# Optimization experiments

Measured on AMD Instinct MI355X. Metric: run time of the kernel, lower is better.

The kernel has to match this reference:

```python
import jax, jax.numpy as jnp
import numpy as np

N = 32768      # tokens
E = 2048       # embedding_dim
V = 256        # vq_dim
K = 256        # codebook size (levels=[256] -> single level, log2 K = 8)
HID = 1024     # condition MLP hidden dim
LOG2K = 8      # log2_num_embeddings
N_MID = 4      # condition_layer - 2 middle blocks
BN_EPS = 1e-5


def _normalize(x):
    return x / (jnp.linalg.norm(x, axis=-1, keepdims=True) + 1e-6)


def _bn(x, g, b):
    # BatchNorm1d, training-mode batch statistics over the codebook rows
    m = x.mean(0)
    v = x.var(0)
    return g * (x - m) * jax.lax.rsqrt(v + BN_EPS) + b


def _codebook(w0, b0, g0, be0, wm, bm, gm, bem, wL, bL):
    # get_bvectors(8, 256): binary expansion of 0..255, width 8 (no pad needed)
    ints = jnp.arange(K)
    bits = ((ints[:, None] >> jnp.arange(LOG2K - 1, -1, -1)[None, :]) & 1).astype(jnp.float32)
    x = jax.nn.relu(_bn(bits @ w0 + b0, g0, be0))
    for i in range(N_MID):
        x = jax.nn.relu(_bn(x @ wm[i] + bm[i], gm[i], bem[i]))
    return x @ wL + bL  # [K, V]


def setup_inputs() -> dict:
    key = jax.random.key(0)
    ks = jax.random.split(key, 8)
    def lin(k, fan_in, shape):
        return (jax.random.normal(k, shape, jnp.float32) / np.sqrt(fan_in)).astype(jnp.float32)
    return {
        "h_in": jax.random.normal(ks[0], (N, E), jnp.float32),
        "temp": jnp.array([0.3], jnp.float32),
        "proj_w": lin(ks[1], E, (E, V)), "proj_b": jnp.zeros((V,), jnp.float32),
        "pinv_w": lin(ks[2], V, (V, E)), "pinv_b": jnp.zeros((E,), jnp.float32),
        "w0": lin(ks[3], LOG2K, (LOG2K, HID)), "b0": jnp.zeros((HID,), jnp.float32),
        "g0": jnp.ones((HID,), jnp.float32), "be0": jnp.zeros((HID,), jnp.float32),
        "wm": lin(ks[4], HID, (N_MID, HID, HID)), "bm": jnp.zeros((N_MID, HID), jnp.float32),
        "gm": jnp.ones((N_MID, HID), jnp.float32), "bem": jnp.zeros((N_MID, HID), jnp.float32),
        "wL": lin(ks[5], HID, (HID, V)), "bL": jnp.zeros((V,), jnp.float32),
    }


def reference(h_in, temp, proj_w, proj_b, pinv_w, pinv_b,
              w0, b0, g0, be0, wm, bm, gm, bem, wL, bL):
    # forward(h_in, mode='eval', temperature=1, level=256); levels=[256] -> idx_all=1
    h = _normalize(h_in @ proj_w + proj_b)                          # proj + sphere normalize, [N, V]
    embed = _normalize(_codebook(w0, b0, g0, be0, wm, bm, gm, bem, wL, bL))  # [K, V]

    # attention(): distance logits with temperature-scaled detached term
    sim = h @ embed.T                                               # [N, K]
    alpha = 1.0 / temp ** 2
    distances = -2.0 * (alpha - 1.0) * jax.lax.stop_gradient(sim) - 2.0 * sim
    A = jax.nn.softmax(-distances, axis=1)                          # [N, K]

    k_code, k_p = jax.random.split(jax.random.key(42))
    code = jax.random.categorical(k_code, -distances, axis=-1)      # multinomial(A, 1), [N]
    onehot = jax.nn.one_hot(code, K, dtype=A.dtype)
    c = onehot * (1.0 - A) + (1.0 - onehot) * (-A)
    A2 = A + jax.lax.stop_gradient(c)                               # fwd value == onehot
    h_vq = h + A2 @ embed - jax.lax.stop_gradient(h)                # straight-through quantize
    vq_loss = jnp.linalg.norm(h_vq - h, axis=-1).mean()             # idx_all == 1

    # select = (0 < p) & (p < 1) since idx=0, idx_all=1
    p = jax.random.uniform(k_p, (h.shape[0],))
    select = (0.0 < p) & (p < 1.0)
    quantized = h_vq * select[:, None].astype(h_vq.dtype)
    probs = A * select[:, None].astype(A.dtype)
    vq_code = code * select.astype(code.dtype)

    quantized_inv = quantized @ pinv_w + pinv_b                     # [N, E]
    return quantized_inv, vq_code, quantized, probs, vq_loss
```

## Files before the change

### kernel.cpp

```cpp
#include <hip/hip_runtime.h>
#include <hip/hip_bf16.h>
#include <stdint.h>
#include <stddef.h>

#ifndef PARTITIONABLE
#define PARTITIONABLE 1
#endif

typedef __attribute__((ext_vector_type(8))) short short8;
typedef __attribute__((ext_vector_type(4))) short short4v;
typedef __attribute__((ext_vector_type(4))) float f32x4;

__host__ __device__ __forceinline__ uint32_t rotl32(uint32_t x, int d){ return (x<<d)|(x>>(32-d)); }

__host__ __device__ __forceinline__ void tf4(uint32_t&x0, uint32_t&x1, int r0,int r1,int r2,int r3){
  x0+=x1; x1=rotl32(x1,r0); x1^=x0;
  x0+=x1; x1=rotl32(x1,r1); x1^=x0;
  x0+=x1; x1=rotl32(x1,r2); x1^=x0;
  x0+=x1; x1=rotl32(x1,r3); x1^=x0;
}
__host__ __device__ __forceinline__ void threefry2x32(uint32_t k0,uint32_t k1,uint32_t x0,uint32_t x1,
                                                      uint32_t&y0,uint32_t&y1){
  uint32_t ks2 = k0^k1^0x1BD11BDAu;
  x0+=k0; x1+=k1;
  tf4(x0,x1,13,15,26,6);  x0+=k1;  x1+=ks2+1u;
  tf4(x0,x1,17,29,16,24); x0+=ks2; x1+=k0+2u;
  tf4(x0,x1,13,15,26,6);  x0+=k0;  x1+=k1+3u;
  tf4(x0,x1,17,29,16,24); x0+=k1;  x1+=ks2+4u;
  tf4(x0,x1,13,15,26,6);  x0+=ks2; x1+=k0+5u;
  y0=x0; y1=x1;
}

__device__ __forceinline__ uint32_t random_bits32(uint32_t k0,uint32_t k1,uint32_t idx, uint32_t half){
#if PARTITIONABLE
  uint32_t y0,y1; threefry2x32(k0,k1, 0u, idx, y0,y1);
  (void)half;
  return y0 ^ y1;
#else
  uint32_t y0,y1;
  if (idx < half) { threefry2x32(k0,k1, idx, idx+half, y0,y1); return y0; }
  else            { threefry2x32(k0,k1, idx-half, idx, y0,y1); return y1; }
#endif
}

__device__ __forceinline__ unsigned short bf16_rne(float x){
  unsigned u = __float_as_uint(x);
  unsigned r = (u + 0x7FFFu + ((u>>16)&1u)) >> 16;
  return (unsigned short)r;
}
__device__ __forceinline__ float bf16_tof(unsigned short h){
  return __uint_as_float(((unsigned)h)<<16);
}
__device__ __forceinline__ void split8(const float* src, short8& hi, short8& lo){
  #pragma unroll
  for (int e=0;e<8;e++){
    unsigned short h = bf16_rne(src[e]);
    hi[e] = (short)h;
    lo[e] = (short)bf16_rne(src[e] - bf16_tof(h));
  }
}
__device__ __forceinline__ void split4(const float* src, short4v& hi, short4v& lo){
  #pragma unroll
  for (int e=0;e<4;e++){
    unsigned short h = bf16_rne(src[e]);
    hi[e] = (short)h;
    lo[e] = (short)bf16_rne(src[e] - bf16_tof(h));
  }
}

__device__ __forceinline__ void gll16(const void* g, void* l){
  __builtin_amdgcn_global_load_lds(
      (const __attribute__((address_space(1))) unsigned int*)g,
      (__attribute__((address_space(3))) unsigned int*)l, 16, 0, 0);
}

__device__ __forceinline__ void mk1_gemm(const float* __restrict__ A, int lda,
                                         const unsigned short* __restrict__ packB,
                                         int K, char* smem, f32x4 (&acc)[2][4]){
  const int tid=threadIdx.x, lane=tid&63, wv=tid>>6;
  const int wr=wv>>2, wc=wv&3;
  const int arow=tid>>3, aseg=tid&7, swA=(arow>>1)&3;
  unsigned short* Ahi=(unsigned short*)smem;
  unsigned short* Alo=(unsigned short*)(smem+4096);
  unsigned short* Bhi=(unsigned short*)(smem+8192);
  unsigned short* Blo=(unsigned short*)(smem+24576);
  const int NT=K/32;
  const int sA = arow*32 + ((aseg>>1)^swA)*8 + (aseg&1)*4;
  const int seg = wv*2;

  float4 av = *(const float4*)(A + (size_t)arow*lda + aseg*4);
  for(int t=0;t<NT;t++){
    __syncthreads();
    {
      float af[4]={av.x,av.y,av.z,av.w}; short4v vh,vl; split4(af,vh,vl);
      *(short4v*)&Ahi[sA]=vh; *(short4v*)&Alo[sA]=vl;
      const unsigned short* src = packB + (size_t)t*16384;
      #pragma unroll
      for(int q=0;q<2;q++){
        gll16(src + (seg+q)*512 + lane*8,        (char*)Bhi + (seg+q)*1024);
        gll16(src + 8192 + (seg+q)*512 + lane*8, (char*)Blo + (seg+q)*1024);
      }
      if (t+1<NT) av = *(const float4*)(A + (size_t)arow*lda + (t+1)*32 + aseg*4);
    }
    __syncthreads();
    short8 ah[2],al[2],bh[4],bl[4];
    const int kg=lane>>4;
    #pragma unroll
    for(int i=0;i<2;i++){
      const int r = wr*32 + i*16 + (lane&15);
      const int offA = r*32 + ((kg ^ ((r>>1)&3))*8);
      ah[i]=*(const short8*)&Ahi[offA]; al[i]=*(const short8*)&Alo[offA];
    }
    #pragma unroll
    for(int j=0;j<4;j++){
      const int c = wc*64 + j*16 + (lane&15);
      const int offB = c*32 + ((kg ^ ((c>>1)&3))*8);
      bh[j]=*(const short8*)&Bhi[offB]; bl[j]=*(const short8*)&Blo[offB];
    }
    #pragma unroll
    for(int i=0;i<2;i++)
      #pragma unroll
      for(int j=0;j<4;j++){
        acc[i][j]=__builtin_amdgcn_mfma_f32_16x16x32_bf16(ah[i],bh[j],acc[i][j],0,0,0);
        acc[i][j]=__builtin_amdgcn_mfma_f32_16x16x32_bf16(ah[i],bl[j],acc[i][j],0,0,0);
        acc[i][j]=__builtin_amdgcn_mfma_f32_16x16x32_bf16(al[i],bh[j],acc[i][j],0,0,0);
      }
  }
}

__global__ __launch_bounds__(256) void pack_w_kernel(const float* __restrict__ W,
                                                     unsigned short* __restrict__ pack){
  const int t = blockIdx.x>>2, s = blockIdx.x&3, c = threadIdx.x;
  const int g = s ^ ((c>>1)&3);
  const float* p = W + (size_t)(t*32 + g*8)*256 + c;
  float bf[8];
  #pragma unroll
  for(int e=0;e<8;e++) bf[e]=p[(size_t)e*256];
  short8 h,l; split8(bf,h,l);
  unsigned short* dst = pack + (size_t)t*16384 + c*32 + s*8;
  *(short8*)dst = h;
  *(short8*)(dst+8192) = l;
}

__device__ __forceinline__ void bn_block_t(float (&acc)[4], int col0,
                                           const float* __restrict__ gma,
                                           const float* __restrict__ bta,
                                           float* __restrict__ Yt,
                                           float* Zs, float* red, float* mcol, float* vcol){
  const int r = threadIdx.x;
  #pragma unroll
  for (int j=0;j<4;j++) Zs[r*5+j] = acc[j];
  __syncthreads();
  if (r < 16){
    const int rl = r & 3, j = r >> 2;
    float s = 0.f;
    for (int rr=rl; rr<256; rr+=4) s += Zs[rr*5+j];
    red[rl*4+j] = s;
  }
  __syncthreads();
  if (r < 4)
    mcol[r] = (red[0*4+r]+red[1*4+r]+red[2*4+r]+red[3*4+r]) * (1.0f/256.0f);
  __syncthreads();
  if (r < 16){
    const int rl = r & 3, j = r >> 2;
    const float m = mcol[j];
    float s2 = 0.f;
    for (int rr=rl; rr<256; rr+=4){ float d = Zs[rr*5+j]-m; s2 += d*d; }
    red[rl*4+j] = s2;
  }
  __syncthreads();
  if (r < 4)
    vcol[r] = (red[0*4+r]+red[1*4+r]+red[2*4+r]+red[3*4+r]) * (1.0f/256.0f);
  __syncthreads();
  #pragma unroll
  for (int j=0;j<4;j++){
    const int c = col0 + j;
    const float scale = gma[c] * rsqrtf(vcol[j] + 1e-5f);
    const float sh = bta[c];
    const float v = (acc[j]-mcol[j])*scale + sh;
    Yt[(size_t)c*256 + r] = v > 0.f ? v : 0.f;
  }
}

__global__ __launch_bounds__(256) void mlp_layer_kernel(
    const float* __restrict__ Xt, const float* __restrict__ W,
    const float* __restrict__ bias,
    const float* __restrict__ gma, const float* __restrict__ bta,
    float* __restrict__ Yt){
  __shared__ float Ws[1024*4];
  __shared__ float Zs[256*5];
  __shared__ float red[16], mcol[4], vcol[4];
  const int r = threadIdx.x;
  const int col0 = blockIdx.x*4;
  #pragma unroll
  for (int q=0;q<4;q++){
    const int k = q*256 + r;
    const float4 wv = *(const float4*)&W[(size_t)k*1024 + col0];
    *(float4*)&Ws[k*4] = wv;
  }
  __syncthreads();
  float acc[4] = {0.f,0.f,0.f,0.f};
  #pragma unroll 8
  for (int k=0;k<1024;k++){
    const float a = Xt[(size_t)k*256 + r];
    const float4 wv = *(const float4*)&Ws[k*4];
    acc[0] += a*wv.x; acc[1] += a*wv.y; acc[2] += a*wv.z; acc[3] += a*wv.w;
  }
  #pragma unroll
  for (int j=0;j<4;j++) acc[j] += bias[col0+j];
  bn_block_t(acc, col0, gma, bta, Yt, Zs, red, mcol, vcol);
}

__global__ __launch_bounds__(256) void mlp_l0t_kernel(
    const float* __restrict__ w0, const float* __restrict__ b0,
    const float* __restrict__ g0, const float* __restrict__ be0,
    float* __restrict__ Yt){
  __shared__ float Zs[256*5];
  __shared__ float red[16], mcol[4], vcol[4];
  const int i = threadIdx.x;
  const int col0 = blockIdx.x*4;
  float acc[4];
  #pragma unroll
  for (int j=0;j<4;j++) acc[j] = b0[col0+j];
  #pragma unroll
  for (int jj=0;jj<8;jj++){
    if ((i >> (7-jj)) & 1){
      #pragma unroll
      for (int j=0;j<4;j++) acc[j] += w0[jj*1024 + col0 + j];
    }
  }
  bn_block_t(acc, col0, g0, be0, Yt, Zs, red, mcol, vcol);
}

__global__ __launch_bounds__(256) void mlp_tail_kernel(
    const float* __restrict__ Xt,
    const float* __restrict__ wL, const float* __restrict__ bL,
    const float* __restrict__ pinv_w, const float* __restrict__ pinv_b,
    float* __restrict__ embed, unsigned short* __restrict__ packE,
    float* __restrict__ Epp){
  __shared__ float xrow[1024];
  __shared__ float erow[256];
  __shared__ float wsum[4];
  const int n = blockIdx.x, t = threadIdx.x;
  #pragma unroll
  for (int q=0;q<4;q++) xrow[q*256+t] = Xt[(size_t)(q*256+t)*256 + n];
  __syncthreads();
  float acc = 0.f;
  #pragma unroll 8
  for (int k=0;k<1024;k++) acc += xrow[k] * wL[(size_t)k*256 + t];
  acc += bL[t];
  const int lane = t & 63, wv = t >> 6;
  float v = acc*acc;
  #pragma unroll
  for (int o=32;o;o>>=1) v += __shfl_xor(v,o);
  if (lane==0) wsum[wv]=v;
  __syncthreads();
  const float total = wsum[0]+wsum[1]+wsum[2]+wsum[3];
  const float inv = 1.0f/(sqrtf(total)+1e-6f);
  const float y = acc*inv;
  embed[(size_t)n*256+t] = y;
  erow[t] = y;
  {
    unsigned short h = bf16_rne(y);
    unsigned short l = bf16_rne(y - bf16_tof(h));
    const int tt=t>>5, kk=t&31, g=kk>>3, e=kk&7, s=g^((n>>1)&3);
    unsigned short* d = packE + (size_t)tt*16384 + n*32 + s*8 + e;
    d[0] = h; d[8192] = l;
  }
  __syncthreads();
  float a8[8] = {0.f,0.f,0.f,0.f,0.f,0.f,0.f,0.f};
  #pragma unroll 4
  for (int k=0;k<256;k++){
    const float ev = erow[k];
    const float4 w0v = *(const float4*)&pinv_w[(size_t)k*2048 + t*8];
    const float4 w1v = *(const float4*)&pinv_w[(size_t)k*2048 + t*8 + 4];
    a8[0] += ev*w0v.x; a8[1] += ev*w0v.y; a8[2] += ev*w0v.z; a8[3] += ev*w0v.w;
    a8[4] += ev*w1v.x; a8[5] += ev*w1v.y; a8[6] += ev*w1v.z; a8[7] += ev*w1v.w;
  }
  #pragma unroll
  for (int j=0;j<8;j++) a8[j] += pinv_b[t*8+j];
  float4* dst = (float4*)(Epp + (size_t)n*2048 + t*8);
  dst[0] = (float4){a8[0],a8[1],a8[2],a8[3]};
  dst[1] = (float4){a8[4],a8[5],a8[6],a8[7]};
}

__global__ __launch_bounds__(512) void proj_norm_kernel(
    const float* __restrict__ A, const unsigned short* __restrict__ packW,
    const float* __restrict__ bias, float* __restrict__ Hn, int K){
  __shared__ char smem[40960];
  f32x4 acc[2][4];
  #pragma unroll
  for (int i=0;i<2;i++)
    #pragma unroll
    for (int j=0;j<4;j++) acc[i][j] = (f32x4){0.f,0.f,0.f,0.f};
  const int bm = blockIdx.x * 64;
  mk1_gemm(A + (size_t)bm*K, K, packW, K, smem, acc);
  __syncthreads();

  const int tid = threadIdx.x, lane = tid&63, wv = tid>>6;
  const int wr = wv>>2, wc = wv&3;
  float* ns = (float*)smem;
  #pragma unroll
  for (int j=0;j<4;j++){
    const int c = wc*64 + j*16 + (lane&15);
    const float bb = bias[c];
    #pragma unroll
    for (int i=0;i<2;i++)
      #pragma unroll
      for (int reg=0;reg<4;reg++) acc[i][j][reg] += bb;
  }
  #pragma unroll
  for (int i=0;i<2;i++)
    #pragma unroll
    for (int reg=0;reg<4;reg++){
      float p = acc[i][0][reg]*acc[i][0][reg] + acc[i][1][reg]*acc[i][1][reg]
              + acc[i][2][reg]*acc[i][2][reg] + acc[i][3][reg]*acc[i][3][reg];
      #pragma unroll
      for (int o=1;o<16;o<<=1) p += __shfl_xor(p, o);
      if ((lane&15)==0) ns[wc*64 + wr*32 + i*16 + (lane>>4)*4 + reg] = p;
    }
  __syncthreads();
  #pragma unroll
  for (int i=0;i<2;i++){
    const int rl = wr*32 + i*16 + (lane>>4)*4;
    #pragma unroll
    for (int reg=0;reg<4;reg++){
      const int r = rl + reg;
      const float tot = ns[0*64+r]+ns[1*64+r]+ns[2*64+r]+ns[3*64+r];
      const float inv = 1.0f/(sqrtf(tot)+1e-6f);
      const size_t grow = (size_t)(bm + r);
      #pragma unroll
      for (int j=0;j<4;j++){
        const int c = wc*64 + j*16 + (lane&15);
        Hn[grow*256 + c] = acc[i][j][reg]*inv;
      }
    }
  }
}

__global__ __launch_bounds__(512) void sim_sample_kernel(
    const float* __restrict__ Hn, const unsigned short* __restrict__ packE,
    const float* __restrict__ embed, const float* __restrict__ temp,
    float* __restrict__ probs, float* __restrict__ codef,
    float* __restrict__ quant, float* __restrict__ norms,
    const float* __restrict__ Epp, const float* __restrict__ pinv_b,
    float* __restrict__ q_inv,
    uint32_t kc0, uint32_t kc1, uint32_t kp0, uint32_t kp1){
  __shared__ char smem[40960];
  f32x4 acc[2][4];
  #pragma unroll
  for (int i=0;i<2;i++)
    #pragma unroll
    for (int j=0;j<4;j++) acc[i][j] = (f32x4){0.f,0.f,0.f,0.f};
  const int bm = blockIdx.x * 64;
  mk1_gemm(Hn + (size_t)bm*256, 256, packE, 256, smem, acc);
  __syncthreads();

  float* redf = (float*)smem;
  int*   redi = (int*)(smem+1024);
  float* smax = (float*)(smem+2048);
  float* ssum = (float*)(smem+2304);
  float* ssel = (float*)(smem+2560);
  int*  scode = (int*)(smem+2816);

  const int tid = threadIdx.x, lane = tid&63, wv = tid>>6;
  const int wr = wv>>2, wc = wv&3;
  const float tv = temp[0];
  const float alpha = 1.0f/(tv*tv);
  #pragma unroll
  for (int i=0;i<2;i++)
    #pragma unroll
    for (int j=0;j<4;j++)
      #pragma unroll
      for (int reg=0;reg<4;reg++){
        const float s = acc[i][j][reg];
        const float dist = -2.0f*(alpha-1.0f)*s - 2.0f*s;
        acc[i][j][reg] = -dist;
      }
  #pragma unroll
  for (int i=0;i<2;i++)
    #pragma unroll
    for (int reg=0;reg<4;reg++){
      float m = fmaxf(fmaxf(acc[i][0][reg], acc[i][1][reg]),
                      fmaxf(acc[i][2][reg], acc[i][3][reg]));
      #pragma unroll
      for (int o=1;o<16;o<<=1) m = fmaxf(m, __shfl_xor(m, o));
      if ((lane&15)==0) redf[wc*64 + wr*32 + i*16 + (lane>>4)*4 + reg] = m;
    }
  __syncthreads();
  if (tid < 64)
    smax[tid] = fmaxf(fmaxf(redf[0*64+tid], redf[1*64+tid]), fmaxf(redf[2*64+tid], redf[3*64+tid]));
  __syncthreads();
  #pragma unroll
  for (int i=0;i<2;i++)
    #pragma unroll
    for (int reg=0;reg<4;reg++){
      const int r = wr*32 + i*16 + (lane>>4)*4 + reg;
      const float m = smax[r];
      float p = expf(acc[i][0][reg]-m) + expf(acc[i][1][reg]-m)
              + expf(acc[i][2][reg]-m) + expf(acc[i][3][reg]-m);
      #pragma unroll
      for (int o=1;o<16;o<<=1) p += __shfl_xor(p, o);
      if ((lane&15)==0) redf[wc*64 + r] = p;
    }
  __syncthreads();
  if (tid < 64){
    ssum[tid] = redf[0*64+tid]+redf[1*64+tid]+redf[2*64+tid]+redf[3*64+tid];
    const uint32_t pb = random_bits32(kp0,kp1,(uint32_t)(bm+tid), 16384u);
    const float pf = __uint_as_float((pb>>9) | 0x3f800000u) - 1.0f;
    ssel[tid] = (pf > 0.0f) ? 1.0f : 0.0f;
  }
  __syncthreads();
  #pragma unroll
  for (int i=0;i<2;i++)
    #pragma unroll
    for (int reg=0;reg<4;reg++){
      const int r = wr*32 + i*16 + (lane>>4)*4 + reg;
      const uint32_t grow = (uint32_t)(bm + r);
      float zb = -1e38f; int ib = 0x7fffffff;
      #pragma unroll
      for (int j=0;j<4;j++){
        const int c = wc*64 + j*16 + (lane&15);
        const uint32_t bits = random_bits32(kc0,kc1, grow*256u + (uint32_t)c, 4194304u);
        const float f = __uint_as_float((bits>>9) | 0x3f800000u) - 1.0f;
        const float TINY = 1.17549435082228751e-38f;
        const float u = fmaxf(TINY, f + TINY);
        const float g = -logf(-logf(u));
        const float z = acc[i][j][reg] + g;
        if (z > zb || (z == zb && c < ib)){ zb = z; ib = c; }
      }
      #pragma unroll
      for (int o=1;o<16;o<<=1){
        const float zo = __shfl_xor(zb, o); const int io = __shfl_xor(ib, o);
        if (zo > zb || (zo == zb && io < ib)){ zb = zo; ib = io; }
      }
      if ((lane&15)==0){ redf[wc*64 + r] = zb; redi[wc*64 + r] = ib; }
    }
  __syncthreads();
  if (tid < 64){
    float zb = redf[0*64+tid]; int ib = redi[0*64+tid];
    #pragma unroll
    for (int w=1; w<4; w++)
      if (redf[w*64+tid] > zb || (redf[w*64+tid] == zb && redi[w*64+tid] < ib)){
        zb = redf[w*64+tid]; ib = redi[w*64+tid];
      }
    scode[tid] = ib;
  }
  __syncthreads();
  #pragma unroll
  for (int i=0;i<2;i++)
    #pragma unroll
    for (int reg=0;reg<4;reg++){
      const int r = wr*32 + i*16 + (lane>>4)*4 + reg;
      const size_t grow = (size_t)(bm + r);
      const float m = smax[r], sum = ssum[r], sel = ssel[r];
      const int code = scode[r];
      float p2 = 0.f;
      #pragma unroll
      for (int j=0;j<4;j++){
        const int c = wc*64 + j*16 + (lane&15);
        const float e = expf(acc[i][j][reg] - m);
        probs[grow*256 + c] = (e/sum) * sel;
        const float ev = embed[(size_t)code*256 + c];
        quant[grow*256 + c] = ev * sel;
        const float d = ev - Hn[grow*256 + c];
        p2 += d*d;
      }
      #pragma unroll
      for (int o=1;o<16;o<<=1) p2 += __shfl_xor(p2, o);
      if ((lane&15)==0) redf[wc*64 + r] = p2;
    }
  __syncthreads();
  if (tid < 64){
    norms[bm+tid] = sqrtf(redf[0*64+tid]+redf[1*64+tid]+redf[2*64+tid]+redf[3*64+tid]);
    codef[bm+tid] = (float)scode[tid] * ssel[tid];
  }
  #pragma unroll
  for (int rr=0; rr<8; rr++){
    const int r = wv*8 + rr;
    const int code = scode[r];
    const float sel = ssel[r];
    const float4* s4 = (const float4*)((sel != 0.0f) ? (Epp + (size_t)code*2048) : pinv_b);
    float4* dst = (float4*)(q_inv + (size_t)(bm + r)*2048);
    #pragma unroll
    for (int q=0;q<8;q++) dst[q*64 + lane] = s4[q*64 + lane];
  }
}

__global__ __launch_bounds__(256) void loss_kernel(const float* __restrict__ norms,
                                                   float* __restrict__ outp){
  const int t = threadIdx.x;
  float s = 0.f;
  for (int i=t;i<32768;i+=256) s += norms[i];
  #pragma unroll
  for (int o=32;o;o>>=1) s += __shfl_xor(s,o);
  __shared__ float wred[4];
  if ((t&63)==0) wred[t>>6]=s;
  __syncthreads();
  if (t==0) outp[0] = (wred[0]+wred[1]+wred[2]+wred[3]) * (1.0f/32768.0f);
}

extern "C" void kernel_launch(void* const* d_in, const int* in_sizes, int n_in,
                              void* d_out, int out_size, void* d_ws, size_t ws_size,
                              hipStream_t stream){
  const float* h_in  = (const float*)d_in[0];
  const float* temp  = (const float*)d_in[1];
  const float* proj_w= (const float*)d_in[2];
  const float* proj_b= (const float*)d_in[3];
  const float* pinv_w= (const float*)d_in[4];
  const float* pinv_b= (const float*)d_in[5];
  const float* w0 = (const float*)d_in[6];
  const float* b0 = (const float*)d_in[7];
  const float* g0 = (const float*)d_in[8];
  const float* be0= (const float*)d_in[9];
  const float* wm = (const float*)d_in[10];
  const float* bm = (const float*)d_in[11];
  const float* gm = (const float*)d_in[12];
  const float* bem= (const float*)d_in[13];
  const float* wL = (const float*)d_in[14];
  const float* bL = (const float*)d_in[15];

  float* out = (float*)d_out;
  float* q_inv  = out;
  float* o_code = out + 67108864;
  float* o_quant= out + 67141632;
  float* o_probs= out + 75530240;
  float* o_loss = out + 83918848;

  float* ws = (float*)d_ws;
  float* Hn     = ws + 0;
  float* XtA    = ws + 8388608;
  float* XtB    = ws + 8650752;
  float* embed  = ws + 8912896;
  float* norms  = ws + 8978432;
  float* Epp    = ws + 9076736;
  unsigned short* packW = (unsigned short*)(ws + 9601024);
  unsigned short* packE = (unsigned short*)(ws + 10125312);

  uint32_t kc0,kc1,kp0,kp1;
#if PARTITIONABLE
  threefry2x32(0u,42u, 0u,0u, kc0,kc1);
  threefry2x32(0u,42u, 0u,1u, kp0,kp1);
#else
  { uint32_t a0,b0w,a1,b1w;
    threefry2x32(0u,42u, 0u,2u, a0,b0w);
    threefry2x32(0u,42u, 1u,3u, a1,b1w);
    kc0=a0; kc1=a1; kp0=b0w; kp1=b1w; }
#endif

  pack_w_kernel<<<256,256,0,stream>>>(proj_w, packW);

  proj_norm_kernel<<<512,512,0,stream>>>(h_in, packW, proj_b, Hn, 2048);

  mlp_l0t_kernel<<<256,256,0,stream>>>(w0, b0, g0, be0, XtA);
  mlp_layer_kernel<<<256,256,0,stream>>>(XtA, wm + 0*1048576, bm + 0*1024, gm + 0*1024, bem + 0*1024, XtB);
  mlp_layer_kernel<<<256,256,0,stream>>>(XtB, wm + 1*1048576, bm + 1*1024, gm + 1*1024, bem + 1*1024, XtA);
  mlp_layer_kernel<<<256,256,0,stream>>>(XtA, wm + 2*1048576, bm + 2*1024, gm + 2*1024, bem + 2*1024, XtB);
  mlp_layer_kernel<<<256,256,0,stream>>>(XtB, wm + 3*1048576, bm + 3*1024, gm + 3*1024, bem + 3*1024, XtA);
  mlp_tail_kernel<<<256,256,0,stream>>>(XtA, wL, bL, pinv_w, pinv_b, embed, packE, Epp);

  sim_sample_kernel<<<512,512,0,stream>>>(Hn, packE, embed, temp,
                                          o_probs, o_code, o_quant, norms,
                                          Epp, pinv_b, q_inv,
                                          kc0,kc1,kp0,kp1);
  loss_kernel<<<1,256,0,stream>>>(norms, o_loss);
}
```

Measured before the change: 586.0 us.

## Widen MLP mid-layer tiles to 16 columns and fuse weight packing with layer 0

Merges the proj weight packing kernel with the first codebook MLP layer to save a launch. Mid MLP layers now compute 16 output columns per block instead of 4, reusing each Xt load across more columns and reducing grid size from 256 to 64 blocks. Tail kernel loop unroll factors are raised. The larger tile reduces redundant activation reads but leaves many CUs idle and raises per-thread register use.

```diff
diff --git a/kernel.cpp b/kernel.cpp
--- a/kernel.cpp
+++ b/kernel.cpp
@@ -128,20 +128,6 @@
   }
 }
 
-__global__ __launch_bounds__(256) void pack_w_kernel(const float* __restrict__ W,
-                                                     unsigned short* __restrict__ pack){
-  const int t = blockIdx.x>>2, s = blockIdx.x&3, c = threadIdx.x;
-  const int g = s ^ ((c>>1)&3);
-  const float* p = W + (size_t)(t*32 + g*8)*256 + c;
-  float bf[8];
-  #pragma unroll
-  for(int e=0;e<8;e++) bf[e]=p[(size_t)e*256];
-  short8 h,l; split8(bf,h,l);
-  unsigned short* dst = pack + (size_t)t*16384 + c*32 + s*8;
-  *(short8*)dst = h;
-  *(short8*)(dst+8192) = l;
-}
-
 __device__ __forceinline__ void bn_block_t(float (&acc)[4], int col0,
                                            const float* __restrict__ gma,
                                            const float* __restrict__ bta,
@@ -182,54 +168,98 @@
   }
 }
 
-__global__ __launch_bounds__(256) void mlp_layer_kernel(
+__global__ __launch_bounds__(256) void prep_kernel(
+    const float* __restrict__ proj_w, unsigned short* __restrict__ packW,
+    const float* __restrict__ w0, const float* __restrict__ b0,
+    const float* __restrict__ g0, const float* __restrict__ be0,
+    float* __restrict__ XtA){
+  __shared__ float Zs[256*5];
+  __shared__ float red[16], mcol[4], vcol[4];
+  const int b = blockIdx.x, tid = threadIdx.x;
+  {
+    const int t = b>>2, s = b&3, c = tid;
+    const int g = s ^ ((c>>1)&3);
+    const float* p = proj_w + (size_t)(t*32 + g*8)*256 + c;
+    float bf[8];
+    #pragma unroll
+    for(int e=0;e<8;e++) bf[e]=p[(size_t)e*256];
+    short8 h,l; split8(bf,h,l);
+    unsigned short* dst = packW + (size_t)t*16384 + c*32 + s*8;
+    *(short8*)dst = h;
+    *(short8*)(dst+8192) = l;
+  }
+  {
+    const int col0 = b*4;
+    float acc[4];
+    #pragma unroll
+    for (int j=0;j<4;j++) acc[j] = b0[col0+j];
+    #pragma unroll
+    for (int jj=0;jj<8;jj++){
+      if ((tid >> (7-jj)) & 1){
+        #pragma unroll
+        for (int j=0;j<4;j++) acc[j] += w0[jj*1024 + col0 + j];
+      }
+    }
+    bn_block_t(acc, col0, g0, be0, XtA, Zs, red, mcol, vcol);
+  }
+}
+
+__global__ __launch_bounds__(256) void mid16_kernel(
     const float* __restrict__ Xt, const float* __restrict__ W,
     const float* __restrict__ bias,
     const float* __restrict__ gma, const float* __restrict__ bta,
     float* __restrict__ Yt){
-  __shared__ float Ws[1024*4];
-  __shared__ float Zs[256*5];
-  __shared__ float red[16], mcol[4], vcol[4];
+  __shared__ float Ws[1024*16];
+  __shared__ float Zs[256*17];
+  __shared__ float red[64], mcol[16], vcol[16];
   const int r = threadIdx.x;
-  const int col0 = blockIdx.x*4;
-  #pragma unroll
-  for (int q=0;q<4;q++){
-    const int k = q*256 + r;
-    const float4 wv = *(const float4*)&W[(size_t)k*1024 + col0];
-    *(float4*)&Ws[k*4] = wv;
-  }
-  __syncthreads();
-  float acc[4] = {0.f,0.f,0.f,0.f};
+  const int c0 = blockIdx.x*16;
+  #pragma unroll
+  for (int idx = r; idx < 4096; idx += 256){
+    const int row = idx>>2, seg = idx&3;
+    *(float4*)&Ws[row*16 + seg*4] = *(const float4*)&W[(size_t)row*1024 + c0 + seg*4];
+  }
+  __syncthreads();
+  float acc[16];
+  #pragma unroll
+  for (int j=0;j<16;j++) acc[j]=0.f;
   #pragma unroll 8
   for (int k=0;k<1024;k++){
     const float a = Xt[(size_t)k*256 + r];
-    const float4 wv = *(const float4*)&Ws[k*4];
-    acc[0] += a*wv.x; acc[1] += a*wv.y; acc[2] += a*wv.z; acc[3] += a*wv.w;
-  }
-  #pragma unroll
-  for (int j=0;j<4;j++) acc[j] += bias[col0+j];
-  bn_block_t(acc, col0, gma, bta, Yt, Zs, red, mcol, vcol);
-}
-
-__global__ __launch_bounds__(256) void mlp_l0t_kernel(
-    const float* __restrict__ w0, const float* __restrict__ b0,
-    const float* __restrict__ g0, const float* __restrict__ be0,
-    float* __restrict__ Yt){
-  __shared__ float Zs[256*5];
-  __shared__ float red[16], mcol[4], vcol[4];
-  const int i = threadIdx.x;
-  const int col0 = blockIdx.x*4;
-  float acc[4];
-  #pragma unroll
-  for (int j=0;j<4;j++) acc[j] = b0[col0+j];
-  #pragma unroll
-  for (int jj=0;jj<8;jj++){
-    if ((i >> (7-jj)) & 1){
-      #pragma unroll
-      for (int j=0;j<4;j++) acc[j] += w0[jj*1024 + col0 + j];
-    }
-  }
-  bn_block_t(acc, col0, g0, be0, Yt, Zs, red, mcol, vcol);
+    #pragma unroll
+    for (int j=0;j<16;j++) acc[j] += a*Ws[k*16+j];
+  }
+  #pragma unroll
+  for (int j=0;j<16;j++) acc[j] += bias[c0+j];
+  #pragma unroll
+  for (int j=0;j<16;j++) Zs[r*17+j] = acc[j];
+  __syncthreads();
+  if (r < 64){
+    const int rl = r & 3, j = r >> 2;
+    float s=0.f;
+    for (int rr=rl; rr<256; rr+=4) s += Zs[rr*17+j];
+    red[rl*16+j] = s;
+  }
+  __syncthreads();
+  if (r < 16) mcol[r] = (red[0*16+r]+red[1*16+r]+red[2*16+r]+red[3*16+r])*(1.0f/256.0f);
+  __syncthreads();
+  if (r < 64){
+    const int rl = r & 3, j = r >> 2;
+    const float m = mcol[j];
+    float s2=0.f;
+    for (int rr=rl; rr<256; rr+=4){ float d=Zs[rr*17+j]-m; s2+=d*d; }
+    red[rl*16+j] = s2;
+  }
+  __syncthreads();
+  if (r < 16) vcol[r] = (red[0*16+r]+red[1*16+r]+red[2*16+r]+red[3*16+r])*(1.0f/256.0f);
+  __syncthreads();
+  #pragma unroll
+  for (int j=0;j<16;j++){
+    const int c = c0+j;
+    const float scale = gma[c]*rsqrtf(vcol[j]+1e-5f);
+    const float v = (acc[j]-mcol[j])*scale + bta[c];
+    Yt[(size_t)c*256 + r] = v>0.f ? v : 0.f;
+  }
 }
 
 __global__ __launch_bounds__(256) void mlp_tail_kernel(
@@ -246,7 +276,7 @@
   for (int q=0;q<4;q++) xrow[q*256+t] = Xt[(size_t)(q*256+t)*256 + n];
   __syncthreads();
   float acc = 0.f;
-  #pragma unroll 8
+  #pragma unroll 16
   for (int k=0;k<1024;k++) acc += xrow[k] * wL[(size_t)k*256 + t];
   acc += bL[t];
   const int lane = t & 63, wv = t >> 6;
@@ -269,7 +299,7 @@
   }
   __syncthreads();
   float a8[8] = {0.f,0.f,0.f,0.f,0.f,0.f,0.f,0.f};
-  #pragma unroll 4
+  #pragma unroll 8
   for (int k=0;k<256;k++){
     const float ev = erow[k];
     const float4 w0v = *(const float4*)&pinv_w[(size_t)k*2048 + t*8];
@@ -548,15 +578,14 @@
     kc0=a0; kc1=a1; kp0=b0w; kp1=b1w; }
 #endif
 
-  pack_w_kernel<<<256,256,0,stream>>>(proj_w, packW);
+  prep_kernel<<<256,256,0,stream>>>(proj_w, packW, w0, b0, g0, be0, XtA);
 
   proj_norm_kernel<<<512,512,0,stream>>>(h_in, packW, proj_b, Hn, 2048);
 
-  mlp_l0t_kernel<<<256,256,0,stream>>>(w0, b0, g0, be0, XtA);
-  mlp_layer_kernel<<<256,256,0,stream>>>(XtA, wm + 0*1048576, bm + 0*1024, gm + 0*1024, bem + 0*1024, XtB);
-  mlp_layer_kernel<<<256,256,0,stream>>>(XtB, wm + 1*1048576, bm + 1*1024, gm + 1*1024, bem + 1*1024, XtA);
-  mlp_layer_kernel<<<256,256,0,stream>>>(XtA, wm + 2*1048576, bm + 2*1024, gm + 2*1024, bem + 2*1024, XtB);
-  mlp_layer_kernel<<<256,256,0,stream>>>(XtB, wm + 3*1048576, bm + 3*1024, gm + 3*1024, bem + 3*1024, XtA);
+  mid16_kernel<<<64,256,0,stream>>>(XtA, wm + 0*1048576, bm + 0*1024, gm + 0*1024, bem + 0*1024, XtB);
+  mid16_kernel<<<64,256,0,stream>>>(XtB, wm + 1*1048576, bm + 1*1024, gm + 1*1024, bem + 1*1024, XtA);
+  mid16_kernel<<<64,256,0,stream>>>(XtA, wm + 2*1048576, bm + 2*1024, gm + 2*1024, bem + 2*1024, XtB);
+  mid16_kernel<<<64,256,0,stream>>>(XtB, wm + 3*1048576, bm + 3*1024, gm + 3*1024, bem + 3*1024, XtA);
   mlp_tail_kernel<<<256,256,0,stream>>>(XtA, wL, bL, pinv_w, pinv_b, embed, packE, Epp);
 
   sim_sample_kernel<<<512,512,0,stream>>>(Hn, packE, embed, temp,
```

Result: slower. 650.2 us (+11.0%).
